# Optimization experiments

Measured on AMD Instinct MI355X. Metric: run time of the kernel, lower is better.

## Reference

```python
import jax, jax.numpy as jnp
import numpy as np

H, M, K, V = 16, 1024, 64, 64
B, Q, T = 2, 2048, 2048


def masked_softmax(x, active, axis):
    # Matches jax.nn.softmax(x, axis=axis, where=active, initial=0.0):
    # max over active entries with an initial value of 0.0; inactive -> prob 0.
    m = jnp.max(jnp.where(active, x, -jnp.inf), axis=axis, keepdims=True)
    m = jnp.maximum(m, 0.0)  # initial=0.0
    e = jnp.where(active, jnp.exp(x - m), 0.0)
    return e / jnp.sum(e, axis=axis, keepdims=True)


def setup_inputs() -> dict:
    key = jax.random.key(0)
    k1, k2, k3, k4, k5, k6, k7 = jax.random.split(key, 7)
    mscale = 1.0 / np.sqrt(M)
    vscale = 1.0 / np.sqrt(V)
    return {
        "qinput": jax.random.normal(k1, (B, Q, M), jnp.float32),
        "kvinput": jax.random.normal(k2, (B, T, M), jnp.float32),
        "qtmask": jax.random.randint(k3, (B, Q, T), 0, 2, jnp.int32),
        "wq": jax.random.normal(k4, (H, M, K), jnp.float32) * mscale,
        "wk": jax.random.normal(k5, (H, M, K), jnp.float32) * mscale,
        "wv": jax.random.normal(k6, (H, M, V), jnp.float32) * mscale,
        "wo": jax.random.normal(k7, (H, V, M), jnp.float32) * vscale,
    }


def reference(qinput, kvinput, qtmask, wq, wk, wv, wo):
    kscale = 1.0 / np.sqrt(K)
    query = jnp.einsum('hmd,bqm->bhqd', wq, qinput)
    key_ = jnp.einsum('hmd,btm->bhtd', wk, kvinput)
    val = jnp.einsum('hmd,btm->bhtd', wv, kvinput)
    alogit = jnp.einsum('bhqd,bhtd->bhqt', query, key_)
    active = jnp.broadcast_to(jnp.logical_not(qtmask)[:, None, :, :], alogit.shape)
    att = masked_softmax(alogit * kscale, active, axis=3)  # bhqt
    pre = jnp.einsum('bhqt,bhtd->bhqd', att, val)
    out = jnp.einsum('hdm,bhqd->bqm', wo, pre)
    return (out, att)
```

## Files before the change

kernel.cpp:

```cpp
#include <hip/hip_runtime.h>

typedef _Float16 f16;
typedef __attribute__((ext_vector_type(4))) _Float16 f16x4;
typedef __attribute__((ext_vector_type(8))) _Float16 f16x8;
typedef __attribute__((ext_vector_type(4))) float f32x4;

#define GLDS16(gp, lp)                                                        \
  __builtin_amdgcn_global_load_lds(                                           \
      (const __attribute__((address_space(1))) void*)(gp),                    \
      (__attribute__((address_space(3))) void*)(lp), 16, 0, 0)

__device__ __forceinline__ f32x4 mfma16(f16x8 a, f16x8 b, f32x4 c) {
  return __builtin_amdgcn_mfma_f32_16x16x32_f16(a, b, c, 0, 0, 0);
}

__global__ __launch_bounds__(256) void k_prep(
    const float* __restrict__ qin, const float* __restrict__ kvin,
    const int* __restrict__ qt, const float* __restrict__ wq,
    const float* __restrict__ wk, const float* __restrict__ wv,
    const float* __restrict__ wo, f16* __restrict__ Xq, f16* __restrict__ Xkv,
    unsigned* __restrict__ Mb, f16* __restrict__ WqT, f16* __restrict__ WkT,
    f16* __restrict__ WvT, f16* __restrict__ WoT) {
  __shared__ float tile[64][65];
  const int bx = blockIdx.x, tid = threadIdx.x;
  if (bx < 8192) {
    const float* s = bx < 4096 ? qin : kvin;
    f16* d = bx < 4096 ? Xq : Xkv;
    const float sc = bx < 4096 ? 0.18033688f : 1.0f;
    int i = ((bx & 4095) * 256 + tid) * 4;
    float4 v = *(const float4*)(s + i);
    f16x4 h;
    h[0] = (f16)(v.x * sc); h[1] = (f16)(v.y * sc);
    h[2] = (f16)(v.z * sc); h[3] = (f16)(v.w * sc);
    *(f16x4*)(d + i) = h;
    return;
  }
  if (bx < 9216) {
    int w = (bx - 8192) * 256 + tid;
    const int* p = qt + (long)w * 32;
    unsigned m = 0;
#pragma unroll
    for (int j4 = 0; j4 < 8; ++j4) {
      int4 v = *(const int4*)(p + j4 * 4);
      m |= (v.x == 0 ? 1u : 0u) << (j4 * 4 + 0);
      m |= (v.y == 0 ? 1u : 0u) << (j4 * 4 + 1);
      m |= (v.z == 0 ? 1u : 0u) << (j4 * 4 + 2);
      m |= (v.w == 0 ? 1u : 0u) << (j4 * 4 + 3);
    }
    Mb[w] = m;
    return;
  }
  int sgt = bx - 9216, which = sgt >> 8, t = sgt & 255;
  const float* src;
  f16* dst;
  int sldr, r0, c0;
  const int dldr = 1024;
  if (which == 0) {
    src = wq + (long)(t >> 4) * 65536; dst = WqT + (long)(t >> 4) * 65536;
    sldr = 64; r0 = (t & 15) * 64; c0 = 0;
  } else if (which == 1) {
    src = wk + (long)(t >> 4) * 65536; dst = WkT + (long)(t >> 4) * 65536;
    sldr = 64; r0 = (t & 15) * 64; c0 = 0;
  } else if (which == 2) {
    src = wv + (long)(t >> 4) * 65536; dst = WvT + (long)(t >> 4) * 65536;
    sldr = 64; r0 = (t & 15) * 64; c0 = 0;
  } else {
    src = wo; dst = WoT;
    sldr = 1024; r0 = (t >> 4) * 64; c0 = (t & 15) * 64;
  }
  int r = tid >> 2, cq = (tid & 3) * 16;
#pragma unroll
  for (int j = 0; j < 16; j += 4) {
    float4 v = *(const float4*)(src + (long)(r0 + r) * sldr + c0 + cq + j);
    tile[r][cq + j] = v.x; tile[r][cq + j + 1] = v.y;
    tile[r][cq + j + 2] = v.z; tile[r][cq + j + 3] = v.w;
  }
  __syncthreads();
  int c = tid >> 2, rq = (tid & 3) * 16;
  f16x8 h0, h1;
#pragma unroll
  for (int j = 0; j < 8; ++j) h0[j] = (f16)tile[rq + j][c];
#pragma unroll
  for (int j = 0; j < 8; ++j) h1[j] = (f16)tile[rq + 8 + j][c];
  f16* dp = dst + (long)(c0 + c) * dldr + r0 + rq;
  *(f16x8*)dp = h0;
  *(f16x8*)(dp + 8) = h1;
}

__device__ __forceinline__ void gemm_body(const f16* __restrict__ A,
                                          const f16* __restrict__ Bt,
                                          void* __restrict__ Cout, int Kd,
                                          int N, int bxx, int byy, int mode,
                                          f16* Al, f16* Bl) {
  const int tid = threadIdx.x, l = tid & 63, w = tid >> 6;
  const int wm = w >> 1, wn = w & 1;
  const int m0 = byy * 128, n0 = bxx * 128;
  const int lr = l >> 2;
  const int lc = (l & 3) * 8;
  const int fr = l & 15;
  const int fk = (l >> 4) * 8;
  f32x4 acc[4][4] = {};
  for (int k0 = 0; k0 < Kd; k0 += 32) {
#pragma unroll
    for (int rd = 0; rd < 2; ++rd) {
      GLDS16(A + (long)(m0 + rd * 64 + w * 16 + lr) * Kd + k0 + lc,
             (char*)Al + rd * 4096 + w * 1024);
      GLDS16(Bt + (long)(n0 + rd * 64 + w * 16 + lr) * Kd + k0 + lc,
             (char*)Bl + rd * 4096 + w * 1024);
    }
    __syncthreads();
    f16x8 af[4], bf[4];
#pragma unroll
    for (int i = 0; i < 4; ++i) {
      af[i] = *(const f16x8*)(Al + (wm * 64 + i * 16 + fr) * 32 + fk);
      bf[i] = *(const f16x8*)(Bl + (wn * 64 + i * 16 + fr) * 32 + fk);
    }
#pragma unroll
    for (int i = 0; i < 4; ++i)
#pragma unroll
      for (int j = 0; j < 4; ++j)
        acc[i][j] = mfma16(af[i], bf[j], acc[i][j]);
    __syncthreads();
  }
  const int rb = (l >> 4) * 4;
#pragma unroll
  for (int i = 0; i < 4; ++i)
#pragma unroll
    for (int j = 0; j < 4; ++j) {
      int row = m0 + wm * 64 + i * 16 + rb;
      int col = n0 + wn * 64 + j * 16 + fr;
      if (mode == 2) {
        int col2 = col - 1024;
        long off = (long)(row >> 11) * 2097152 + (long)col2 * 2048 +
                   (row & 2047);
        f16x4 o;
        o[0] = (f16)acc[i][j][0]; o[1] = (f16)acc[i][j][1];
        o[2] = (f16)acc[i][j][2]; o[3] = (f16)acc[i][j][3];
        *(f16x4*)((f16*)Cout + off) = o;
      } else {
#pragma unroll
        for (int r = 0; r < 4; ++r) {
          if (mode == 1)
            ((float*)Cout)[(long)(row + r) * N + col] = acc[i][j][r];
          else
            ((f16*)Cout)[(long)(row + r) * N + col] = (f16)acc[i][j][r];
        }
      }
    }
}

__global__ __launch_bounds__(256) void k_gemm_qkv(
    const f16* __restrict__ Xq, const f16* __restrict__ WqT,
    f16* __restrict__ Qm, const f16* __restrict__ Xkv,
    const f16* __restrict__ WkT, f16* __restrict__ KVm,
    f16* __restrict__ Vt) {
  __shared__ __attribute__((aligned(16))) f16 Al[128 * 32];
  __shared__ __attribute__((aligned(16))) f16 Bl[128 * 32];
  if (blockIdx.x < 8) {
    gemm_body(Xq, WqT, (void*)Qm, 1024, 1024, blockIdx.x, blockIdx.y, 0, Al,
              Bl);
  } else {
    int bxx = blockIdx.x - 8;
    if (bxx < 8)
      gemm_body(Xkv, WkT, (void*)KVm, 1024, 2048, bxx, blockIdx.y, 0, Al, Bl);
    else
      gemm_body(Xkv, WkT, (void*)Vt, 1024, 2048, bxx, blockIdx.y, 2, Al, Bl);
  }
}

__global__ __launch_bounds__(256) void k_gemm_out(const f16* __restrict__ Pre,
                                                  const f16* __restrict__ WoT,
                                                  float* __restrict__ out) {
  __shared__ __attribute__((aligned(16))) f16 Al[128 * 32];
  __shared__ __attribute__((aligned(16))) f16 Bl[128 * 32];
  gemm_body(Pre, WoT, (void*)out, 1024, 1024, blockIdx.x, blockIdx.y, 1, Al,
            Bl);
}

__global__ __launch_bounds__(256) void k_attn(
    const f16* __restrict__ Qm, const f16* __restrict__ Km,
    const f16* __restrict__ Vt, const unsigned* __restrict__ mb,
    float* __restrict__ att, f16* __restrict__ Pre, int ldk) {
  __shared__ unsigned mloc[16 * 68];
  __shared__ float wsum[4][16];
  __shared__ __attribute__((aligned(16))) f16 ebuf[4][16 * 136];
  const int qt = blockIdx.x, h = blockIdx.y, b = blockIdx.z;
  const int q0 = qt * 16;
  const int tid = threadIdx.x, l = tid & 63, w = tid >> 6;
  const int fr = l & 15, fg = l >> 4;

  for (int i = tid; i < 1024; i += 256)
    mloc[(i >> 6) * 68 + (i & 63)] =
        mb[(long)(b * 2048 + q0 + (i >> 6)) * 64 + (i & 63)];

  const f16* qb = Qm + (long)(b * 2048 + q0 + fr) * 1024 + h * 64 + fg * 8;
  f16x8 qf0 = *(const f16x8*)qb;
  f16x8 qf1 = *(const f16x8*)(qb + 32);
  __syncthreads();

  const f16* kb = Km + (long)(b * 2048 + w * 512 + fr) * ldk + h * 64 + fg * 8;
  f16x8 ka0[2], ka1[2];
#pragma unroll
  for (int p = 0; p < 2; ++p) {
    ka0[p] = *(const f16x8*)(kb + (long)p * 16 * ldk);
    ka1[p] = *(const f16x8*)(kb + (long)p * 16 * ldk + 32);
  }
  f16x4 s16[32];
  float sm[4] = {0.f, 0.f, 0.f, 0.f};
#pragma unroll
  for (int i = 0; i < 32; ++i) {
    f16x8 k0 = ka0[i & 1], k1 = ka1[i & 1];
    if (i < 30) {
      ka0[i & 1] = *(const f16x8*)(kb + (long)(i + 2) * 16 * ldk);
      ka1[i & 1] = *(const f16x8*)(kb + (long)(i + 2) * 16 * ldk + 32);
    }
    f32x4 s = {};
    s = mfma16(k0, qf0, s);
    s = mfma16(k1, qf1, s);
    unsigned bits =
        (mloc[fr * 68 + w * 16 + (i >> 1)] >> ((i & 1) * 16 + fg * 4)) & 0xFu;
    f16x4 e4;
#pragma unroll
    for (int r = 0; r < 4; ++r) {
      float ev = ((bits >> r) & 1) ? __builtin_amdgcn_exp2f(s[r]) : 0.f;
      sm[r] += ev;
      e4[r] = (f16)ev;
    }
    s16[i] = e4;
  }
  float sa = (sm[0] + sm[1]) + (sm[2] + sm[3]);
  sa += __shfl_xor(sa, 16, 64);
  sa += __shfl_xor(sa, 32, 64);
  if (l < 16) wsum[w][fr] = sa;

  f16* eb = ebuf[w];
  const f16* vb =
      Vt + ((long)((b * 16 + h) * 64 + fr)) * 2048 + w * 512 + fg * 8;
  f32x4 pacc[4] = {};
#pragma unroll
  for (int c = 0; c < 4; ++c) {
#pragma unroll
    for (int i2 = 0; i2 < 8; ++i2)
      *(f16x4*)(eb + fr * 136 + i2 * 16 + fg * 4) = s16[c * 8 + i2];
#pragma unroll
    for (int kt = 0; kt < 4; ++kt) {
      f16x8 af = *(const f16x8*)(eb + fr * 136 + kt * 32 + fg * 8);
      __builtin_amdgcn_s_setprio(1);
#pragma unroll
      for (int vt = 0; vt < 4; ++vt) {
        f16x8 bf =
            *(const f16x8*)(vb + (long)vt * 16 * 2048 + c * 128 + kt * 32);
        pacc[vt] = mfma16(af, bf, pacc[vt]);
      }
      __builtin_amdgcn_s_setprio(0);
    }
  }

  float* pp = (float*)eb;
#pragma unroll
  for (int vt = 0; vt < 4; ++vt)
#pragma unroll
    for (int r = 0; r < 4; ++r)
      pp[(fg * 4 + r) * 64 + vt * 16 + fr] = pacc[vt][r];
  __syncthreads();

  {
    const int q = tid >> 4, v4 = (tid & 15) * 4;
    float totq = (wsum[0][q] + wsum[1][q]) + (wsum[2][q] + wsum[3][q]);
    float ri = 1.f / totq;
    f32x4 p4 = {0.f, 0.f, 0.f, 0.f};
#pragma unroll
    for (int w4 = 0; w4 < 4; ++w4) {
      f32x4 t4 = *(const f32x4*)((const float*)ebuf[w4] + q * 64 + v4);
      p4 += t4;
    }
    f16x4 o;
    o[0] = (f16)(p4[0] * ri);
    o[1] = (f16)(p4[1] * ri);
    o[2] = (f16)(p4[2] * ri);
    o[3] = (f16)(p4[3] * ri);
    *(f16x4*)(Pre + (long)(b * 2048 + q0 + q) * 1024 + h * 64 + v4) = o;
  }

  {
    float tot = (wsum[0][fr] + wsum[1][fr]) + (wsum[2][fr] + wsum[3][fr]);
    float rinv = 1.f / tot;
    float* ao =
        att + (long)((b * 16 + h) * 2048 + q0 + fr) * 2048 + w * 512 + fg * 4;
#pragma unroll
    for (int i = 0; i < 32; ++i) {
      f16x4 e4 = s16[i];
      f32x4 o;
      o[0] = (float)e4[0] * rinv;
      o[1] = (float)e4[1] * rinv;
      o[2] = (float)e4[2] * rinv;
      o[3] = (float)e4[3] * rinv;
      __builtin_nontemporal_store(o, (f32x4*)(ao + i * 16));
    }
  }
}

extern "C" void kernel_launch(void* const* d_in, const int* in_sizes, int n_in,
                              void* d_out, int out_size, void* d_ws,
                              size_t ws_size, hipStream_t stream) {
  const float* qinput = (const float*)d_in[0];
  const float* kvinput = (const float*)d_in[1];
  const int* qtmask = (const int*)d_in[2];
  const float* wq = (const float*)d_in[3];
  const float* wk = (const float*)d_in[4];
  const float* wv = (const float*)d_in[5];
  const float* wo = (const float*)d_in[6];
  float* out = (float*)d_out;
  float* att = out + (long)2 * 2048 * 1024;

  char* ws = (char*)d_ws;
  f16* Xq = (f16*)(ws);
  f16* Xkv = (f16*)(ws + 8388608);
  f16* WqT = (f16*)(ws + 16777216);
  f16* WkT = (f16*)(ws + 18874368);
  f16* WvT = (f16*)(ws + 20971520);
  f16* WoT = (f16*)(ws + 23068672);
  f16* Qm = (f16*)(ws + 25165824);
  f16* KVm = (f16*)(ws + 33554432);
  f16* Vt = (f16*)(ws + 50331648);
  f16* Pre = (f16*)(ws + 58720256);
  unsigned* Mb = (unsigned*)(ws + 67108864);

  k_prep<<<dim3(10240), dim3(256), 0, stream>>>(qinput, kvinput, qtmask, wq,
                                                wk, wv, wo, Xq, Xkv, Mb, WqT,
                                                WkT, WvT, WoT);
  k_gemm_qkv<<<dim3(24, 32), dim3(256), 0, stream>>>(Xq, WqT, Qm, Xkv, WkT,
                                                     KVm, Vt);
  k_attn<<<dim3(128, 16, 2), dim3(256), 0, stream>>>(Qm, KVm, Vt, Mb, att, Pre,
                                                     2048);
  k_gemm_out<<<dim3(8, 32), dim3(256), 0, stream>>>(Pre, WoT, out);
}
```

Baseline: 420.0 us.

## Make attention blocks persistent over query tiles with XCD-aware head mapping

The attention kernel now launches 512 blocks instead of 4096. Each block loops over 8 consecutive 16-row query tiles for one (batch, head), and blocks are mapped so that all blocks for the same head land on the same XCD. The aim is to keep K and V for a head hot in that XCD's L2 and to cut block launch overhead. The trade-offs are fewer concurrent blocks, which can hurt latency hiding, and extra __syncthreads inside the loop. The att stores now come before the PV product.

```diff
diff --git a/kernel.cpp b/kernel.cpp
--- a/kernel.cpp
+++ b/kernel.cpp
@@ -184,107 +184,70 @@
   __shared__ unsigned mloc[16 * 68];
   __shared__ float wsum[4][16];
   __shared__ __attribute__((aligned(16))) f16 ebuf[4][16 * 136];
-  const int qt = blockIdx.x, h = blockIdx.y, b = blockIdx.z;
-  const int q0 = qt * 16;
+  const int id = blockIdx.x;
+  const int xcd = id & 7, local = id >> 3;
+  const int hb = xcd * 4 + (local >> 4);
+  const int qg = local & 15;
+  const int h = hb & 15, b = hb >> 4;
   const int tid = threadIdx.x, l = tid & 63, w = tid >> 6;
   const int fr = l & 15, fg = l >> 4;
 
-  for (int i = tid; i < 1024; i += 256)
-    mloc[(i >> 6) * 68 + (i & 63)] =
-        mb[(long)(b * 2048 + q0 + (i >> 6)) * 64 + (i & 63)];
-
-  const f16* qb = Qm + (long)(b * 2048 + q0 + fr) * 1024 + h * 64 + fg * 8;
-  f16x8 qf0 = *(const f16x8*)qb;
-  f16x8 qf1 = *(const f16x8*)(qb + 32);
-  __syncthreads();
-
-  const f16* kb = Km + (long)(b * 2048 + w * 512 + fr) * ldk + h * 64 + fg * 8;
-  f16x8 ka0[2], ka1[2];
-#pragma unroll
-  for (int p = 0; p < 2; ++p) {
-    ka0[p] = *(const f16x8*)(kb + (long)p * 16 * ldk);
-    ka1[p] = *(const f16x8*)(kb + (long)p * 16 * ldk + 32);
-  }
-  f16x4 s16[32];
-  float sm[4] = {0.f, 0.f, 0.f, 0.f};
-#pragma unroll
-  for (int i = 0; i < 32; ++i) {
-    f16x8 k0 = ka0[i & 1], k1 = ka1[i & 1];
-    if (i < 30) {
-      ka0[i & 1] = *(const f16x8*)(kb + (long)(i + 2) * 16 * ldk);
-      ka1[i & 1] = *(const f16x8*)(kb + (long)(i + 2) * 16 * ldk + 32);
-    }
-    f32x4 s = {};
-    s = mfma16(k0, qf0, s);
-    s = mfma16(k1, qf1, s);
-    unsigned bits =
-        (mloc[fr * 68 + w * 16 + (i >> 1)] >> ((i & 1) * 16 + fg * 4)) & 0xFu;
-    f16x4 e4;
-#pragma unroll
-    for (int r = 0; r < 4; ++r) {
-      float ev = ((bits >> r) & 1) ? __builtin_amdgcn_exp2f(s[r]) : 0.f;
-      sm[r] += ev;
-      e4[r] = (f16)ev;
-    }
-    s16[i] = e4;
-  }
-  float sa = (sm[0] + sm[1]) + (sm[2] + sm[3]);
-  sa += __shfl_xor(sa, 16, 64);
-  sa += __shfl_xor(sa, 32, 64);
-  if (l < 16) wsum[w][fr] = sa;
-
-  f16* eb = ebuf[w];
+  const f16* kb0 = Km + (long)(b * 2048 + w * 512 + fr) * ldk + h * 64 + fg * 8;
   const f16* vb =
       Vt + ((long)((b * 16 + h) * 64 + fr)) * 2048 + w * 512 + fg * 8;
-  f32x4 pacc[4] = {};
-#pragma unroll
-  for (int c = 0; c < 4; ++c) {
-#pragma unroll
-    for (int i2 = 0; i2 < 8; ++i2)
-      *(f16x4*)(eb + fr * 136 + i2 * 16 + fg * 4) = s16[c * 8 + i2];
-#pragma unroll
-    for (int kt = 0; kt < 4; ++kt) {
-      f16x8 af = *(const f16x8*)(eb + fr * 136 + kt * 32 + fg * 8);
-      __builtin_amdgcn_s_setprio(1);
-#pragma unroll
-      for (int vt = 0; vt < 4; ++vt) {
-        f16x8 bf =
-            *(const f16x8*)(vb + (long)vt * 16 * 2048 + c * 128 + kt * 32);
-        pacc[vt] = mfma16(af, bf, pacc[vt]);
-      }
-      __builtin_amdgcn_s_setprio(0);
-    }
-  }
-
-  float* pp = (float*)eb;
-#pragma unroll
-  for (int vt = 0; vt < 4; ++vt)
-#pragma unroll
-    for (int r = 0; r < 4; ++r)
-      pp[(fg * 4 + r) * 64 + vt * 16 + fr] = pacc[vt][r];
-  __syncthreads();
-
-  {
-    const int q = tid >> 4, v4 = (tid & 15) * 4;
-    float totq = (wsum[0][q] + wsum[1][q]) + (wsum[2][q] + wsum[3][q]);
-    float ri = 1.f / totq;
-    f32x4 p4 = {0.f, 0.f, 0.f, 0.f};
-#pragma unroll
-    for (int w4 = 0; w4 < 4; ++w4) {
-      f32x4 t4 = *(const f32x4*)((const float*)ebuf[w4] + q * 64 + v4);
-      p4 += t4;
-    }
-    f16x4 o;
-    o[0] = (f16)(p4[0] * ri);
-    o[1] = (f16)(p4[1] * ri);
-    o[2] = (f16)(p4[2] * ri);
-    o[3] = (f16)(p4[3] * ri);
-    *(f16x4*)(Pre + (long)(b * 2048 + q0 + q) * 1024 + h * 64 + v4) = o;
-  }
-
-  {
+  f16* eb = ebuf[w];
+
+  for (int it = 0; it < 8; ++it) {
+    const int q0 = (qg * 8 + it) * 16;
+    __syncthreads();
+
+    for (int i = tid; i < 1024; i += 256)
+      mloc[(i >> 6) * 68 + (i & 63)] =
+          mb[(long)(b * 2048 + q0 + (i >> 6)) * 64 + (i & 63)];
+
+    const f16* qb = Qm + (long)(b * 2048 + q0 + fr) * 1024 + h * 64 + fg * 8;
+    f16x8 qf0 = *(const f16x8*)qb;
+    f16x8 qf1 = *(const f16x8*)(qb + 32);
+    __syncthreads();
+
+    f16x8 ka0[2], ka1[2];
+#pragma unroll
+    for (int p = 0; p < 2; ++p) {
+      ka0[p] = *(const f16x8*)(kb0 + (long)p * 16 * ldk);
+      ka1[p] = *(const f16x8*)(kb0 + (long)p * 16 * ldk + 32);
+    }
+    f16x4 s16[32];
+    float sm[4] = {0.f, 0.f, 0.f, 0.f};
+#pragma unroll
+    for (int i = 0; i < 32; ++i) {
+      f16x8 k0 = ka0[i & 1], k1 = ka1[i & 1];
+      if (i < 30) {
+        ka0[i & 1] = *(const f16x8*)(kb0 + (long)(i + 2) * 16 * ldk);
+        ka1[i & 1] = *(const f16x8*)(kb0 + (long)(i + 2) * 16 * ldk + 32);
+      }
+      f32x4 s = {};
+      s = mfma16(k0, qf0, s);
+      s = mfma16(k1, qf1, s);
+      unsigned bits =
+          (mloc[fr * 68 + w * 16 + (i >> 1)] >> ((i & 1) * 16 + fg * 4)) &
+          0xFu;
+      f16x4 e4;
+#pragma unroll
+      for (int r = 0; r < 4; ++r) {
+        float ev = ((bits >> r) & 1) ? __builtin_amdgcn_exp2f(s[r]) : 0.f;
+        sm[r] += ev;
+        e4[r] = (f16)ev;
+      }
+      s16[i] = e4;
+    }
+    float sa = (sm[0] + sm[1]) + (sm[2] + sm[3]);
+    sa += __shfl_xor(sa, 16, 64);
+    sa += __shfl_xor(sa, 32, 64);
+    if (l < 16) wsum[w][fr] = sa;
+    __syncthreads();
     float tot = (wsum[0][fr] + wsum[1][fr]) + (wsum[2][fr] + wsum[3][fr]);
-    float rinv = 1.f / tot;
+    const float rinv = 1.f / tot;
+
     float* ao =
         att + (long)((b * 16 + h) * 2048 + q0 + fr) * 2048 + w * 512 + fg * 4;
 #pragma unroll
@@ -296,6 +259,52 @@
       o[2] = (float)e4[2] * rinv;
       o[3] = (float)e4[3] * rinv;
       __builtin_nontemporal_store(o, (f32x4*)(ao + i * 16));
+    }
+
+    f32x4 pacc[4] = {};
+#pragma unroll
+    for (int c = 0; c < 4; ++c) {
+#pragma unroll
+      for (int i2 = 0; i2 < 8; ++i2)
+        *(f16x4*)(eb + fr * 136 + i2 * 16 + fg * 4) = s16[c * 8 + i2];
+#pragma unroll
+      for (int kt = 0; kt < 4; ++kt) {
+        f16x8 af = *(const f16x8*)(eb + fr * 136 + kt * 32 + fg * 8);
+        __builtin_amdgcn_s_setprio(1);
+#pragma unroll
+        for (int vt = 0; vt < 4; ++vt) {
+          f16x8 bf =
+              *(const f16x8*)(vb + (long)vt * 16 * 2048 + c * 128 + kt * 32);
+          pacc[vt] = mfma16(af, bf, pacc[vt]);
+        }
+        __builtin_amdgcn_s_setprio(0);
+      }
+    }
+
+    float* pp = (float*)eb;
+#pragma unroll
+    for (int vt = 0; vt < 4; ++vt)
+#pragma unroll
+      for (int r = 0; r < 4; ++r)
+        pp[(fg * 4 + r) * 64 + vt * 16 + fr] = pacc[vt][r];
+    __syncthreads();
+
+    {
+      const int q = tid >> 4, v4 = (tid & 15) * 4;
+      float totq = (wsum[0][q] + wsum[1][q]) + (wsum[2][q] + wsum[3][q]);
+      float ri = 1.f / totq;
+      f32x4 p4 = {0.f, 0.f, 0.f, 0.f};
+#pragma unroll
+      for (int w4 = 0; w4 < 4; ++w4) {
+        f32x4 t4 = *(const f32x4*)((const float*)ebuf[w4] + q * 64 + v4);
+        p4 += t4;
+      }
+      f16x4 o;
+      o[0] = (f16)(p4[0] * ri);
+      o[1] = (f16)(p4[1] * ri);
+      o[2] = (f16)(p4[2] * ri);
+      o[3] = (f16)(p4[3] * ri);
+      *(f16x4*)(Pre + (long)(b * 2048 + q0 + q) * 1024 + h * 64 + v4) = o;
     }
   }
 }
@@ -331,7 +340,6 @@
                                                 WkT, WvT, WoT);
   k_gemm_qkv<<<dim3(24, 32), dim3(256), 0, stream>>>(Xq, WqT, Qm, Xkv, WkT,
                                                      KVm, Vt);
-  k_attn<<<dim3(128, 16, 2), dim3(256), 0, stream>>>(Qm, KVm, Vt, Mb, att, Pre,
-                                                     2048);
+  k_attn<<<dim3(512), dim3(256), 0, stream>>>(Qm, KVm, Vt, Mb, att, Pre, 2048);
   k_gemm_out<<<dim3(8, 32), dim3(256), 0, stream>>>(Pre, WoT, out);
 }
```

After: 505.2 us. +20.3%, slower.
